# Performance work log

Hardware: AMD Instinct MI355X
Metric: run time of the kernel (lower is better)

Reference implementation:

```python
import jax, jax.numpy as jnp
import numpy as np

NUM_HEADS = 16
HEAD_DIM = 64  # hidden_size // num_heads = 1024 // 16


def setup_inputs() -> dict:
    key = jax.random.key(0)
    ks = jax.random.split(key, 5)
    B, S, D = 4, 2048, 1024
    scale = 1.0 / np.sqrt(D)
    return {
        "hidden_states": jax.random.normal(ks[0], (B, S, D), dtype=jnp.float32),
        "Wq": jax.random.normal(ks[1], (D, D), dtype=jnp.float32) * scale,
        "Wk": jax.random.normal(ks[2], (D, D), dtype=jnp.float32) * scale,
        "Wv": jax.random.normal(ks[3], (D, D), dtype=jnp.float32) * scale,
        "Wo": jax.random.normal(ks[4], (D, D), dtype=jnp.float32) * scale,
    }


def reference(hidden_states, Wq, Wk, Wv, Wo):
    B, S, D = hidden_states.shape
    H, hd = NUM_HEADS, HEAD_DIM
    # torch nn.Linear(y = x @ W.T), bias=False
    q = (hidden_states @ Wq.T).reshape(B, S, H, hd)
    k = (hidden_states @ Wk.T).reshape(B, S, H, hd)
    v = (hidden_states @ Wv.T).reshape(B, S, H, hd)
    q = q / jnp.sqrt(jnp.float32(hd))
    # scores: [B, H, S, S] — module materializes full score matrix
    scores = jnp.einsum("bqhd,bkhd->bhqk", q, k)
    weights = jax.nn.softmax(scores, axis=-1)
    attn = jnp.einsum("bhqk,bkhd->bqhd", weights, v).reshape(B, S, D)
    return attn @ Wo.T
```

## Files before the change

kernel.cpp:

```cpp
#include <hip/hip_runtime.h>

using u16 = unsigned short;
using u32 = unsigned int;
typedef __attribute__((ext_vector_type(8))) short bf16x8;
typedef __attribute__((ext_vector_type(4))) short bf16x4;
typedef __attribute__((ext_vector_type(4))) float f32x4;
typedef __attribute__((ext_vector_type(16))) float f32x16;
typedef __attribute__((ext_vector_type(4))) u32 u32x4;

__device__ __forceinline__ u16 f2bf(float f) {
  u32 u = __builtin_bit_cast(u32, f);
  u += 0x7FFFu + ((u >> 16) & 1u);
  return (u16)(u >> 16);
}

__device__ __forceinline__ void load_lds16(const void* g, void* l) {
  typedef const __attribute__((address_space(1))) u32 GA;
  typedef __attribute__((address_space(3))) u32 LA;
  __builtin_amdgcn_global_load_lds((GA*)g, (LA*)l, 16, 0, 0);
}

__device__ __forceinline__ bf16x4 tr16(const u16* p) {
  typedef __attribute__((address_space(3))) const u16 LT;
  bf16x4 d;
  asm volatile("ds_read_b64_tr_b16 %0, %1" : "=v"(d) : "v"((LT*)p));
  return d;
}

__device__ __forceinline__ float exp2_fast(float x) {
  float r;
  asm("v_exp_f32 %0, %1" : "=v"(r) : "v"(x));
  return r;
}

__device__ __forceinline__ u32 cvt_pk_bf16(float lo, float hi) {
  u32 r;
  asm("v_cvt_pk_bf16_f32 %0, %1, %2" : "=v"(r) : "v"(lo), "v"(hi));
  return r;
}

__device__ __forceinline__ void permlane32_swap(u32& a, u32& b) {
  asm volatile("v_permlane32_swap_b32 %0, %1" : "+v"(a), "+v"(b));
}

__global__ void cvt_all(const float* __restrict__ hs, const float* __restrict__ Wq,
                        const float* __restrict__ Wk, const float* __restrict__ Wv,
                        const float* __restrict__ Wo, u16* __restrict__ hs16,
                        u16* __restrict__ w16, int hs4, int w4seg, float qscale) {
  int i = blockIdx.x * blockDim.x + threadIdx.x;
  const float* src;
  u16* dst;
  float sc = 1.0f;
  int off;
  if (i < hs4) {
    src = hs; dst = hs16; off = i;
  } else {
    int j = i - hs4;
    int seg = j / w4seg;
    off = j - seg * w4seg;
    dst = w16 + (size_t)seg * (size_t)w4seg * 4;
    src = seg == 0 ? Wq : seg == 1 ? Wk : seg == 2 ? Wv : Wo;
    if (seg == 0) sc = qscale;
  }
  float4 v = reinterpret_cast<const float4*>(src)[off];
  ushort4 o;
  o.x = f2bf(v.x * sc);
  o.y = f2bf(v.y * sc);
  o.z = f2bf(v.z * sc);
  o.w = f2bf(v.w * sc);
  reinterpret_cast<ushort4*>(dst)[off] = o;
}

template <typename OutT>
__global__ __launch_bounds__(256, 2) void gemm_bt(
    const u16* __restrict__ A, const u16* __restrict__ Bw,
    OutT* __restrict__ C, int M, int N, int K) {
  __shared__ u16 At[128 * 32];
  __shared__ u16 Bt[128 * 32];
  const int tid = threadIdx.x;
  const int wid = tid >> 6, lane = tid & 63;
  const int wr = wid >> 1, wc = wid & 1;
  const int laneR = lane & 15, laneG = lane >> 4;
  const int laneK = laneG * 8;

  const int nbm = M >> 7;
  const int nbn = N >> 7;
  const int cpx = gridDim.x >> 3;
  const int id = blockIdx.x;
  const int swz = (id & 7) * cpx + (id >> 3);
  const int c = swz / cpx, j = swz % cpx;
  const int rpc = nbm >> 3;
  const int bm = c * rpc + j / nbn;
  const int bn = j % nbn;

  f32x4 acc[4][4];
#pragma unroll
  for (int i = 0; i < 4; ++i)
#pragma unroll
    for (int jj = 0; jj < 4; ++jj) acc[i][jj] = f32x4{0.f, 0.f, 0.f, 0.f};

  const int e0 = tid * 8;
  const int r0 = e0 >> 5, c0 = e0 & 31;
  const u16* Ab = A + (size_t)(bm * 128) * K;
  const u16* Bb = Bw + (size_t)(bn * 128) * K;

  for (int k0 = 0; k0 < K; k0 += 32) {
#pragma unroll
    for (int i = 0; i < 2; ++i) {
      load_lds16(Ab + (size_t)(i * 64 + r0) * K + k0 + c0, &At[(i * 256 + wid * 64) * 8]);
      load_lds16(Bb + (size_t)(i * 64 + r0) * K + k0 + c0, &Bt[(i * 256 + wid * 64) * 8]);
    }
    __syncthreads();
    bf16x8 af[4], bfr[4];
#pragma unroll
    for (int i = 0; i < 4; ++i)
      af[i] = *(const bf16x8*)&At[(wr * 64 + i * 16 + laneR) * 32 + laneK];
#pragma unroll
    for (int jj = 0; jj < 4; ++jj)
      bfr[jj] = *(const bf16x8*)&Bt[(wc * 64 + jj * 16 + laneR) * 32 + laneK];
#pragma unroll
    for (int i = 0; i < 4; ++i)
#pragma unroll
      for (int jj = 0; jj < 4; ++jj)
        acc[i][jj] = __builtin_amdgcn_mfma_f32_16x16x32_bf16(af[i], bfr[jj], acc[i][jj], 0, 0, 0);
    __syncthreads();
  }

  const int crow = bm * 128 + wr * 64;
  const int ccol = bn * 128 + wc * 64;
#pragma unroll
  for (int i = 0; i < 4; ++i)
#pragma unroll
    for (int jj = 0; jj < 4; ++jj)
#pragma unroll
      for (int r = 0; r < 4; ++r) {
        int row = crow + i * 16 + laneG * 4 + r;
        int col = ccol + jj * 16 + laneR;
        float v = acc[i][jj][r];
        if constexpr (sizeof(OutT) == 2)
          C[(size_t)row * N + col] = f2bf(v);
        else
          C[(size_t)row * N + col] = v;
      }
}

template <int MH, int NH>
__device__ __forceinline__ void mfma_quad(f32x4 (&acc)[8][4], bf16x8 (&afr)[4][2],
                                          bf16x8 (&bfr)[2][2]) {
  __builtin_amdgcn_s_setprio(1);
#pragma unroll
  for (int m = 0; m < 4; ++m)
#pragma unroll
    for (int n = 0; n < 2; ++n)
#pragma unroll
      for (int ks = 0; ks < 2; ++ks)
        acc[MH * 4 + m][NH * 2 + n] = __builtin_amdgcn_mfma_f32_16x16x32_bf16(
            afr[m][ks], bfr[n][ks], acc[MH * 4 + m][NH * 2 + n], 0, 0, 0);
  __builtin_amdgcn_s_setprio(0);
}

#define GBAR() __builtin_amdgcn_s_barrier()
#define PWAIT()                                            \
  do {                                                     \
    GBAR();                                                \
    asm volatile("s_waitcnt lgkmcnt(0)" ::: "memory");     \
  } while (0)
#define PWAITV()                                                    \
  do {                                                              \
    GBAR();                                                         \
    asm volatile("s_waitcnt vmcnt(2) lgkmcnt(0)" ::: "memory");     \
  } while (0)

template <typename OutT>
__global__ __launch_bounds__(512, 2) void gemm256(
    const u16* __restrict__ A, const u16* __restrict__ Bw,
    OutT* __restrict__ C, int M, int N, int K) {
  __shared__ __align__(16) char ldsb[131072];
  const int tid = threadIdx.x;
  const int wid = tid >> 6, lane = tid & 63;
  const int wr = wid >> 2, wc = wid & 3;
  const int laneR = lane & 15, laneG = lane >> 4;
  const int swzR = (laneR & 7) << 4;

  const int nbm = M >> 8;
  const int nbn = N >> 8;
  const int cpx = gridDim.x >> 3;
  const int id = blockIdx.x;
  const int swzid = (id & 7) * cpx + (id >> 3);
  const int c = swzid / cpx, j = swzid % cpx;
  const int rpc = nbm >> 3;
  const int bm = c * rpc + j / nbn;
  const int bn = j % nbn;

  const u16* Ab = A + (size_t)(bm * 256) * K;
  const u16* Bb = Bw + (size_t)(bn * 256) * K;

  const int s_r = tid >> 3;
  const int s_k = ((tid & 7) ^ (s_r & 7)) * 8;

  auto stage_half = [&](const u16* Xb, int regio, int buf, int hh, int kt) {
    char* d = ldsb + regio + buf * 32768 + hh * 16384 + wid * 1024;
#pragma unroll
    for (int jj = 0; jj < 2; ++jj)
      load_lds16(Xb + (size_t)(hh * 128 + jj * 64 + s_r) * K + kt * 64 + s_k,
                 d + jj * 8192);
  };
  auto rdA = [&](int buf, int mh, int m, int ks) -> bf16x8 {
    return *(const bf16x8*)(ldsb + buf * 32768 + wr * 16384 +
                            (mh * 64 + m * 16 + laneR) * 128 +
                            ((ks * 64 + laneG * 16) ^ swzR));
  };
  auto rdB = [&](int buf, int nh, int n, int ks) -> bf16x8 {
    return *(const bf16x8*)(ldsb + 65536 + buf * 32768 + (wc >> 1) * 16384 +
                            ((wc & 1) * 64 + nh * 32 + n * 16 + laneR) * 128 +
                            ((ks * 64 + laneG * 16) ^ swzR));
  };

  f32x4 acc[8][4];
#pragma unroll
  for (int i = 0; i < 8; ++i)
#pragma unroll
    for (int jj = 0; jj < 4; ++jj) acc[i][jj] = f32x4{0.f, 0.f, 0.f, 0.f};

  bf16x8 afr[4][2], bfr[2][2];
  auto readAB = [&](int buf, int mh, int nh) {
#pragma unroll
    for (int m = 0; m < 4; ++m) {
      afr[m][0] = rdA(buf, mh, m, 0);
      afr[m][1] = rdA(buf, mh, m, 1);
    }
#pragma unroll
    for (int n = 0; n < 2; ++n) {
      bfr[n][0] = rdB(buf, nh, n, 0);
      bfr[n][1] = rdB(buf, nh, n, 1);
    }
  };
  auto readB = [&](int buf, int nh) {
#pragma unroll
    for (int n = 0; n < 2; ++n) {
      bfr[n][0] = rdB(buf, nh, n, 0);
      bfr[n][1] = rdB(buf, nh, n, 1);
    }
  };

  const int NT = K >> 6, NI = K >> 7;

  stage_half(Ab, 0, 0, 0, 0);
  stage_half(Ab, 0, 0, 1, 0);
  stage_half(Bb, 65536, 0, 0, 0);
  stage_half(Bb, 65536, 0, 1, 0);
  stage_half(Ab, 0, 1, 0, 1);
  asm volatile("s_waitcnt vmcnt(2)" ::: "memory");
  GBAR();

  for (int i = 0; i < NI; ++i) {
    const int t1 = (2 * i + 1) & (NT - 1);
    const int t2 = (2 * i + 2) & (NT - 1);
    const int t3 = (2 * i + 3) & (NT - 1);
    readAB(0, 0, 0); stage_half(Ab, 0, 1, 1, t1); PWAIT();
    mfma_quad<0, 0>(acc, afr, bfr); GBAR();
    readB(0, 1); stage_half(Bb, 65536, 1, 0, t1); PWAIT();
    mfma_quad<0, 1>(acc, afr, bfr); GBAR();
    readAB(0, 1, 0); stage_half(Bb, 65536, 1, 1, t1); PWAIT();
    mfma_quad<1, 0>(acc, afr, bfr); GBAR();
    readB(0, 1); stage_half(Ab, 0, 0, 0, t2); PWAITV();
    mfma_quad<1, 1>(acc, afr, bfr); GBAR();
    readAB(1, 0, 0); stage_half(Ab, 0, 0, 1, t2); PWAIT();
    mfma_quad<0, 0>(acc, afr, bfr); GBAR();
    readB(1, 1); stage_half(Bb, 65536, 0, 0, t2); PWAIT();
    mfma_quad<0, 1>(acc, afr, bfr); GBAR();
    readAB(1, 1, 0); stage_half(Bb, 65536, 0, 1, t2); PWAIT();
    mfma_quad<1, 0>(acc, afr, bfr); GBAR();
    readB(1, 1); stage_half(Ab, 0, 1, 0, t3); PWAITV();
    mfma_quad<1, 1>(acc, afr, bfr); GBAR();
  }

  const int crow = bm * 256 + wr * 128;
  const int ccol = bn * 256 + wc * 64;
#pragma unroll
  for (int mf = 0; mf < 8; ++mf)
#pragma unroll
    for (int nf = 0; nf < 4; ++nf)
#pragma unroll
      for (int r = 0; r < 4; ++r) {
        int row = crow + mf * 16 + laneG * 4 + r;
        int col = ccol + nf * 16 + laneR;
        float v = acc[mf][nf][r];
        if constexpr (sizeof(OutT) == 2)
          C[(size_t)row * N + col] = f2bf(v);
        else
          C[(size_t)row * N + col] = v;
      }
}

__global__ __launch_bounds__(512, 4) void flash_attn(
    const u16* __restrict__ QKV, u16* __restrict__ O) {
  constexpr int S = 2048, DQ = 3072, DO = 1024;
  __shared__ u16 Kt[3][4096];
  __shared__ u16 Vt[3][4096];
  const int tid = threadIdx.x, wid = tid >> 6, lane = tid & 63;
  const int lq = lane & 31, hi = lane >> 5;

  const int id = blockIdx.x;
  const int jj0 = id >> 3;
  const int bh = (id & 7) * 8 + (jj0 >> 3), qt = jj0 & 7;
  const int b = bh >> 4, h = bh & 15;

  const size_t bq = (size_t)b * S * DQ;
  const u16* Qg = QKV + bq + h * 64;
  const u16* Kg = QKV + bq + 1024 + h * 64;
  const u16* Vg = QKV + bq + 2048 + h * 64;
  const int qrow0 = qt * 256 + wid * 32;

  const int k_kv = tid >> 3;
  const int k_col = ((tid & 7) ^ (k_kv & 7)) * 8;
  const int v_kv = ((tid >> 5) << 2) | ((tid >> 1) & 3);
  const int v_hd = (((tid >> 3) & 3) << 4) | ((tid & 1) << 3);

  bf16x8 qf[4];
#pragma unroll
  for (int kc = 0; kc < 4; ++kc)
    qf[kc] = *(const bf16x8*)&Qg[(size_t)(qrow0 + lq) * DQ + kc * 16 + hi * 8];

  f32x16 o0, o1;
#pragma unroll
  for (int r = 0; r < 16; ++r) { o0[r] = 0.f; o1[r] = 0.f; }
  float l = 0.f;

  auto stage = [&](int buf, int kv0) {
    load_lds16(Kg + (size_t)(kv0 + k_kv) * DQ + k_col, &Kt[buf][wid * 512]);
    load_lds16(Vg + (size_t)(kv0 + v_kv) * DQ + v_hd, &Vt[buf][wid * 512]);
  };

  stage(0, 0);
  stage(1, 64);
  asm volatile("s_waitcnt vmcnt(2)" ::: "memory");
  __builtin_amdgcn_s_barrier();
  asm volatile("" ::: "memory");

  int cur = 0, pre = 2;
  for (int t = 0; t < 32; ++t) {
    stage(pre, ((t + 2) & 31) * 64);

    f32x16 st[2];
#pragma unroll
    for (int blk = 0; blk < 2; ++blk) {
#pragma unroll
      for (int r = 0; r < 16; ++r) st[blk][r] = 0.f;
      bf16x8 kf[4];
#pragma unroll
      for (int kc = 0; kc < 4; ++kc) {
        int kv = blk * 32 + lq;
        int byt = kv * 128 + ((kc * 32 + hi * 16) ^ ((kv & 7) << 4));
        kf[kc] = *(const bf16x8*)((const char*)&Kt[cur][0] + byt);
      }
#pragma unroll
      for (int kc = 0; kc < 4; ++kc)
        st[blk] = __builtin_amdgcn_mfma_f32_32x32x16_bf16(kf[kc], qf[kc], st[blk], 0, 0, 0);
    }

    float ps = 0.f;
#pragma unroll
    for (int blk = 0; blk < 2; ++blk)
#pragma unroll
      for (int r = 0; r < 16; ++r) {
        float p = exp2_fast(st[blk][r]);
        st[blk][r] = p;
        ps += p;
      }
    l += ps;

    u32 W0[8], W1[8];
#pragma unroll
    for (int r2 = 0; r2 < 8; ++r2) {
      W0[r2] = cvt_pk_bf16(st[0][2 * r2], st[0][2 * r2 + 1]);
      W1[r2] = cvt_pk_bf16(st[1][2 * r2], st[1][2 * r2 + 1]);
    }
    bf16x8 pb[4];
#pragma unroll
    for (int ks = 0; ks < 2; ++ks) {
      u32 a0 = W0[4 * ks], a2 = W0[4 * ks + 2];
      u32 a1 = W0[4 * ks + 1], a3 = W0[4 * ks + 3];
      permlane32_swap(a0, a2);
      permlane32_swap(a1, a3);
      pb[ks] = __builtin_bit_cast(bf16x8, u32x4{a0, a1, a2, a3});
    }
#pragma unroll
    for (int ks = 0; ks < 2; ++ks) {
      u32 a0 = W1[4 * ks], a2 = W1[4 * ks + 2];
      u32 a1 = W1[4 * ks + 1], a3 = W1[4 * ks + 3];
      permlane32_swap(a0, a2);
      permlane32_swap(a1, a3);
      pb[2 + ks] = __builtin_bit_cast(bf16x8, u32x4{a0, a1, a2, a3});
    }

#pragma unroll
    for (int c2 = 0; c2 < 2; ++c2) {
      bf16x4 vh[4][2];
      const int hb = c2 * 2 + ((lane >> 4) & 1);
#pragma unroll
      for (int ks = 0; ks < 4; ++ks)
#pragma unroll
        for (int p2 = 0; p2 < 2; ++p2) {
          int a = ks * 4 + hi * 2 + p2;
          vh[ks][p2] = tr16(&Vt[cur][(a * 4 + hb) * 64 + (lane & 15) * 4]);
        }
      asm volatile("s_waitcnt lgkmcnt(0)" ::: "memory");
      __builtin_amdgcn_sched_barrier(0);
      f32x16 oc = c2 ? o1 : o0;
#pragma unroll
      for (int ks = 0; ks < 4; ++ks) {
        bf16x8 vf = __builtin_shufflevector(vh[ks][0], vh[ks][1], 0, 1, 2, 3, 4, 5, 6, 7);
        oc = __builtin_amdgcn_mfma_f32_32x32x16_bf16(vf, pb[ks], oc, 0, 0, 0);
      }
      if (c2) o1 = oc; else o0 = oc;
    }

    asm volatile("s_waitcnt vmcnt(2)" ::: "memory");
    __builtin_amdgcn_s_barrier();
    asm volatile("" ::: "memory");

    cur = (cur == 2) ? 0 : cur + 1;
    pre = (pre == 2) ? 0 : pre + 1;
  }

  l += __shfl_xor(l, 32);
  const float inv = 1.0f / l;
  const size_t boo = (size_t)b * S * DO + h * 64;
  const size_t qb = boo + (size_t)(qrow0 + lq) * DO;
#pragma unroll
  for (int r = 0; r < 16; ++r) {
    int hd = (r & 3) + 8 * (r >> 2) + 4 * hi;
    O[qb + hd] = f2bf(o0[r] * inv);
    O[qb + 32 + hd] = f2bf(o1[r] * inv);
  }
}

extern "C" void kernel_launch(void* const* d_in, const int* in_sizes, int n_in,
                              void* d_out, int out_size, void* d_ws, size_t ws_size,
                              hipStream_t stream) {
  const float* hs = (const float*)d_in[0];
  const float* Wq = (const float*)d_in[1];
  const float* Wk = (const float*)d_in[2];
  const float* Wv = (const float*)d_in[3];
  const float* Wo = (const float*)d_in[4];
  float* out = (float*)d_out;

  constexpr int Bn = 4, S = 2048, Dm = 1024;
  constexpr int M = Bn * S;
  constexpr size_t SZ = (size_t)M * Dm;
  constexpr size_t WSZ = (size_t)Dm * Dm;

  u16* wsp = (u16*)d_ws;
  u16* QKVb = wsp;
  u16* hs16 = QKVb + (size_t)M * 3072;
  u16* Ob = hs16;
  u16* W16 = hs16 + SZ;
  u16* Wo16 = W16 + 3 * WSZ;
  (void)ws_size; (void)in_sizes; (void)n_in; (void)out_size;

  constexpr int HS4 = (int)(SZ / 4);
  constexpr int W4SEG = (int)(WSZ / 4);
  cvt_all<<<(HS4 + 4 * W4SEG) / 256, 256, 0, stream>>>(
      hs, Wq, Wk, Wv, Wo, hs16, W16, HS4, W4SEG, 0.125f * 1.44269504f);

  gemm256<u16><<<(M / 256) * (3072 / 256), 512, 0, stream>>>(hs16, W16, QKVb, M, 3072, Dm);

  flash_attn<<<512, 512, 0, stream>>>(QKVb, Ob);

  gemm_bt<float><<<(M / 128) * (Dm / 128), 256, 0, stream>>>(Ob, Wo16, out, M, Dm, Dm);
}
```

Baseline: 185.4 us.

## Replace output projection GEMM with pipelined 256x128 tile kernel

The output projection previously used a simple 128x128 GEMM that loaded one K=32 slice at a time with two barriers per step and no prefetch. It is replaced by a 512-thread 256x128-tile kernel with XOR-swizzled LDS, 64-wide K tiles and a multi-buffer schedule. This schedule issues global-to-LDS loads for later tiles while MFMAs run on the current one, using split waitcnt barriers. The aim is to hide memory latency and raise MFMA utilization. The cost is 96KB of LDS per block, which limits occupancy, and a fragile hand-written wait-count schedule.

Measured after the change: 180.8 us. 2.5% less time.

```diff
diff --git a/kernel.cpp b/kernel.cpp
--- a/kernel.cpp
+++ b/kernel.cpp
@@ -71,94 +71,6 @@
   reinterpret_cast<ushort4*>(dst)[off] = o;
 }
 
-template <typename OutT>
-__global__ __launch_bounds__(256, 2) void gemm_bt(
-    const u16* __restrict__ A, const u16* __restrict__ Bw,
-    OutT* __restrict__ C, int M, int N, int K) {
-  __shared__ u16 At[128 * 32];
-  __shared__ u16 Bt[128 * 32];
-  const int tid = threadIdx.x;
-  const int wid = tid >> 6, lane = tid & 63;
-  const int wr = wid >> 1, wc = wid & 1;
-  const int laneR = lane & 15, laneG = lane >> 4;
-  const int laneK = laneG * 8;
-
-  const int nbm = M >> 7;
-  const int nbn = N >> 7;
-  const int cpx = gridDim.x >> 3;
-  const int id = blockIdx.x;
-  const int swz = (id & 7) * cpx + (id >> 3);
-  const int c = swz / cpx, j = swz % cpx;
-  const int rpc = nbm >> 3;
-  const int bm = c * rpc + j / nbn;
-  const int bn = j % nbn;
-
-  f32x4 acc[4][4];
-#pragma unroll
-  for (int i = 0; i < 4; ++i)
-#pragma unroll
-    for (int jj = 0; jj < 4; ++jj) acc[i][jj] = f32x4{0.f, 0.f, 0.f, 0.f};
-
-  const int e0 = tid * 8;
-  const int r0 = e0 >> 5, c0 = e0 & 31;
-  const u16* Ab = A + (size_t)(bm * 128) * K;
-  const u16* Bb = Bw + (size_t)(bn * 128) * K;
-
-  for (int k0 = 0; k0 < K; k0 += 32) {
-#pragma unroll
-    for (int i = 0; i < 2; ++i) {
-      load_lds16(Ab + (size_t)(i * 64 + r0) * K + k0 + c0, &At[(i * 256 + wid * 64) * 8]);
-      load_lds16(Bb + (size_t)(i * 64 + r0) * K + k0 + c0, &Bt[(i * 256 + wid * 64) * 8]);
-    }
-    __syncthreads();
-    bf16x8 af[4], bfr[4];
-#pragma unroll
-    for (int i = 0; i < 4; ++i)
-      af[i] = *(const bf16x8*)&At[(wr * 64 + i * 16 + laneR) * 32 + laneK];
-#pragma unroll
-    for (int jj = 0; jj < 4; ++jj)
-      bfr[jj] = *(const bf16x8*)&Bt[(wc * 64 + jj * 16 + laneR) * 32 + laneK];
-#pragma unroll
-    for (int i = 0; i < 4; ++i)
-#pragma unroll
-      for (int jj = 0; jj < 4; ++jj)
-        acc[i][jj] = __builtin_amdgcn_mfma_f32_16x16x32_bf16(af[i], bfr[jj], acc[i][jj], 0, 0, 0);
-    __syncthreads();
-  }
-
-  const int crow = bm * 128 + wr * 64;
-  const int ccol = bn * 128 + wc * 64;
-#pragma unroll
-  for (int i = 0; i < 4; ++i)
-#pragma unroll
-    for (int jj = 0; jj < 4; ++jj)
-#pragma unroll
-      for (int r = 0; r < 4; ++r) {
-        int row = crow + i * 16 + laneG * 4 + r;
-        int col = ccol + jj * 16 + laneR;
-        float v = acc[i][jj][r];
-        if constexpr (sizeof(OutT) == 2)
-          C[(size_t)row * N + col] = f2bf(v);
-        else
-          C[(size_t)row * N + col] = v;
-      }
-}
-
-template <int MH, int NH>
-__device__ __forceinline__ void mfma_quad(f32x4 (&acc)[8][4], bf16x8 (&afr)[4][2],
-                                          bf16x8 (&bfr)[2][2]) {
-  __builtin_amdgcn_s_setprio(1);
-#pragma unroll
-  for (int m = 0; m < 4; ++m)
-#pragma unroll
-    for (int n = 0; n < 2; ++n)
-#pragma unroll
-      for (int ks = 0; ks < 2; ++ks)
-        acc[MH * 4 + m][NH * 2 + n] = __builtin_amdgcn_mfma_f32_16x16x32_bf16(
-            afr[m][ks], bfr[n][ks], acc[MH * 4 + m][NH * 2 + n], 0, 0, 0);
-  __builtin_amdgcn_s_setprio(0);
-}
-
 #define GBAR() __builtin_amdgcn_s_barrier()
 #define PWAIT()                                            \
   do {                                                     \
@@ -170,6 +82,26 @@
     GBAR();                                                         \
     asm volatile("s_waitcnt vmcnt(2) lgkmcnt(0)" ::: "memory");     \
   } while (0)
+#define PWAITV4()                                                   \
+  do {                                                              \
+    GBAR();                                                         \
+    asm volatile("s_waitcnt vmcnt(4) lgkmcnt(0)" ::: "memory");     \
+  } while (0)
+
+template <int MH, int NH>
+__device__ __forceinline__ void mfma_quad(f32x4 (&acc)[8][4], bf16x8 (&afr)[4][2],
+                                          bf16x8 (&bfr)[2][2]) {
+  __builtin_amdgcn_s_setprio(1);
+#pragma unroll
+  for (int m = 0; m < 4; ++m)
+#pragma unroll
+    for (int n = 0; n < 2; ++n)
+#pragma unroll
+      for (int ks = 0; ks < 2; ++ks)
+        acc[MH * 4 + m][NH * 2 + n] = __builtin_amdgcn_mfma_f32_16x16x32_bf16(
+            afr[m][ks], bfr[n][ks], acc[MH * 4 + m][NH * 2 + n], 0, 0, 0);
+  __builtin_amdgcn_s_setprio(0);
+}
 
 template <typename OutT>
 __global__ __launch_bounds__(512, 2) void gemm256(
@@ -293,6 +225,139 @@
       }
 }
 
+template <int NH>
+__device__ __forceinline__ void mq(f32x4 (&acc)[4][4], bf16x8 (&afr)[4][2],
+                                   bf16x8 (&bfr)[2][2]) {
+  __builtin_amdgcn_s_setprio(1);
+#pragma unroll
+  for (int m = 0; m < 4; ++m)
+#pragma unroll
+    for (int n = 0; n < 2; ++n)
+#pragma unroll
+      for (int ks = 0; ks < 2; ++ks)
+        acc[m][NH * 2 + n] = __builtin_amdgcn_mfma_f32_16x16x32_bf16(
+            afr[m][ks], bfr[n][ks], acc[m][NH * 2 + n], 0, 0, 0);
+  __builtin_amdgcn_s_setprio(0);
+}
+
+template <typename OutT>
+__global__ __launch_bounds__(512, 2) void gemm256x128(
+    const u16* __restrict__ A, const u16* __restrict__ Bw,
+    OutT* __restrict__ C, int M, int N, int K) {
+  __shared__ __align__(16) char ldsb[98304];
+  const int tid = threadIdx.x;
+  const int wid = tid >> 6, lane = tid & 63;
+  const int wr = wid >> 1, wc = wid & 1;
+  const int laneR = lane & 15, laneG = lane >> 4;
+  const int swzR = (laneR & 7) << 4;
+
+  const int nbm = M >> 8;
+  const int nbn = N >> 7;
+  const int cpx = gridDim.x >> 3;
+  const int id = blockIdx.x;
+  const int swzid = (id & 7) * cpx + (id >> 3);
+  const int c = swzid / cpx, j = swzid % cpx;
+  const int rpc = nbm >> 3;
+  const int bm = c * rpc + j / nbn;
+  const int bn = j % nbn;
+
+  const u16* Ab = A + (size_t)(bm * 256) * K;
+  const u16* Bb = Bw + (size_t)(bn * 128) * K;
+
+  const int s_r = tid >> 3;
+  const int s_k = ((tid & 7) ^ (s_r & 7)) * 8;
+
+  auto stage_unit = [&](const u16* Xb, int dstoff, int row0, int kt) {
+    char* d = ldsb + dstoff + wid * 1024;
+#pragma unroll
+    for (int jj = 0; jj < 2; ++jj)
+      load_lds16(Xb + (size_t)(row0 + jj * 64 + s_r) * K + kt * 64 + s_k,
+                 d + jj * 8192);
+  };
+  auto rdA = [&](int buf, int m, int ks) -> bf16x8 {
+    return *(const bf16x8*)(ldsb + buf * 32768 + (wr >> 1) * 16384 +
+                            ((wr & 1) * 64 + m * 16 + laneR) * 128 +
+                            ((ks * 64 + laneG * 16) ^ swzR));
+  };
+  auto rdB = [&](int buf, int nh, int n, int ks) -> bf16x8 {
+    return *(const bf16x8*)(ldsb + 65536 + buf * 16384 +
+                            (wc * 64 + nh * 32 + n * 16 + laneR) * 128 +
+                            ((ks * 64 + laneG * 16) ^ swzR));
+  };
+
+  f32x4 acc[4][4];
+#pragma unroll
+  for (int i = 0; i < 4; ++i)
+#pragma unroll
+    for (int jj = 0; jj < 4; ++jj) acc[i][jj] = f32x4{0.f, 0.f, 0.f, 0.f};
+
+  bf16x8 afr[4][2], bfr[2][2];
+  auto readA = [&](int buf) {
+#pragma unroll
+    for (int m = 0; m < 4; ++m) {
+      afr[m][0] = rdA(buf, m, 0);
+      afr[m][1] = rdA(buf, m, 1);
+    }
+  };
+  auto readB = [&](int buf, int nh) {
+#pragma unroll
+    for (int n = 0; n < 2; ++n) {
+      bfr[n][0] = rdB(buf, nh, n, 0);
+      bfr[n][1] = rdB(buf, nh, n, 1);
+    }
+  };
+
+  const int NT = K >> 6, NI = K >> 7;
+
+  stage_unit(Ab, 0, 0, 0);
+  stage_unit(Ab, 16384, 128, 0);
+  stage_unit(Bb, 65536, 0, 0);
+  stage_unit(Ab, 32768, 0, 1);
+  asm volatile("s_waitcnt vmcnt(2)" ::: "memory");
+  GBAR();
+
+  for (int i = 0; i < NI; ++i) {
+    const int tb = (2 * i + 1) & (NT - 1);
+    const int tc = (2 * i + 2) & (NT - 1);
+    const int td = (2 * i + 3) & (NT - 1);
+    readA(0); readB(0, 0);
+    stage_unit(Ab, 32768 + 16384, 128, tb);
+    stage_unit(Bb, 65536 + 16384, 0, tb);
+    PWAIT();
+    mq<0>(acc, afr, bfr); GBAR();
+    readB(0, 1);
+    stage_unit(Ab, 0, 0, tc);
+    stage_unit(Ab, 16384, 128, tc);
+    PWAITV4();
+    mq<1>(acc, afr, bfr); GBAR();
+    readA(1); readB(1, 0);
+    stage_unit(Bb, 65536, 0, tc);
+    PWAIT();
+    mq<0>(acc, afr, bfr); GBAR();
+    readB(1, 1);
+    stage_unit(Ab, 32768, 0, td);
+    PWAITV();
+    mq<1>(acc, afr, bfr); GBAR();
+  }
+
+  const int crow = bm * 256 + wr * 64;
+  const int ccol = bn * 128 + wc * 64;
+#pragma unroll
+  for (int mf = 0; mf < 4; ++mf)
+#pragma unroll
+    for (int nf = 0; nf < 4; ++nf)
+#pragma unroll
+      for (int r = 0; r < 4; ++r) {
+        int row = crow + mf * 16 + laneG * 4 + r;
+        int col = ccol + nf * 16 + laneR;
+        float v = acc[mf][nf][r];
+        if constexpr (sizeof(OutT) == 2)
+          C[(size_t)row * N + col] = f2bf(v);
+        else
+          C[(size_t)row * N + col] = v;
+      }
+}
+
 __global__ __launch_bounds__(512, 4) void flash_attn(
     const u16* __restrict__ QKV, u16* __restrict__ O) {
   constexpr int S = 2048, DQ = 3072, DO = 1024;
@@ -468,5 +533,5 @@
 
   flash_attn<<<512, 512, 0, stream>>>(QKVb, Ob);
 
-  gemm_bt<float><<<(M / 128) * (Dm / 128), 256, 0, stream>>>(Ob, Wo16, out, M, Dm, Dm);
-}
+  gemm256x128<float><<<(M / 256) * (Dm / 128), 512, 0, stream>>>(Ob, Wo16, out, M, Dm, Dm);
+}
```
